# Optimization experiments

Measured on AMD Instinct MI355X. Metric: run time of the kernel, lower is better.

Reference implementation:

```python
import jax, jax.numpy as jnp
import numpy as np

NUM_HEADS = 16
ROPE_THETA = 10000.0


def setup_inputs() -> dict:
    key = jax.random.key(0)
    k1, k2, k3 = jax.random.split(key, 3)
    B, T, C = 2, 2048, 1024
    x = jax.random.normal(k1, (B, T, C), dtype=jnp.float32)
    w_qkv = jax.random.normal(k2, (3 * C, C), dtype=jnp.float32) * 0.02
    w_out = jax.random.normal(k3, (C, C), dtype=jnp.float32) * 0.02
    return {"x": x, "w_qkv": w_qkv, "w_out": w_out}


def _apply_rope(x, cos, sin):
    # x: (B, H, T, D); interleaved complex pairs: (x[...,2i], x[...,2i+1])
    B, H, T, D = x.shape
    xp = x.reshape(B, H, T, D // 2, 2)
    xr, xi = xp[..., 0], xp[..., 1]
    # cos/sin: (T, D//2) broadcast over (B, H)
    out_r = xr * cos - xi * sin
    out_i = xr * sin + xi * cos
    return jnp.stack([out_r, out_i], axis=-1).reshape(B, H, T, D)


def reference(x, w_qkv, w_out):
    B, T, C = x.shape
    H = NUM_HEADS
    D = C // H
    scale = 1.0 / np.sqrt(D).astype(np.float32)

    qkv = x @ w_qkv.T                      # (B, T, 3C)
    q, k, v = jnp.split(qkv, 3, axis=-1)

    def to_heads(t):
        return t.reshape(B, T, H, D).transpose(0, 2, 1, 3)  # (B, H, T, D)

    q, k, v = to_heads(q), to_heads(k), to_heads(v)

    # RoPE frequencies: freqs[t, j] = t / theta^(2j/D)
    inv_freq = 1.0 / (ROPE_THETA ** (jnp.arange(0, D, 2, dtype=jnp.float32) / D))
    freqs = jnp.arange(T, dtype=jnp.float32)[:, None] * inv_freq[None, :]  # (T, D//2)
    cos, sin = jnp.cos(freqs), jnp.sin(freqs)

    q = _apply_rope(q, cos, sin)
    k = _apply_rope(k, cos, sin)

    att = jnp.einsum('bhqd,bhkd->bhqk', q, k) * scale   # (B, H, T, T)
    causal = jnp.tril(jnp.ones((T, T), dtype=bool))
    att = jnp.where(causal[None, None], att, -jnp.inf)
    att = jax.nn.softmax(att, axis=-1)
    # dropout p=0.0 (eval) -> identity

    out = jnp.einsum('bhqk,bhkd->bhqd', att, v)          # (B, H, T, D)
    out = out.transpose(0, 2, 1, 3).reshape(B, T, C)
    return out @ w_out.T
```

## Files before the change

kernel.cpp:

```cpp
#include <hip/hip_runtime.h>
#include <hip/hip_bf16.h>
#include <math.h>

#define DEV __device__ __forceinline__

typedef float  floatx4 __attribute__((ext_vector_type(4)));
typedef short  bf16x8  __attribute__((ext_vector_type(8)));
typedef short  bf16x4  __attribute__((ext_vector_type(4)));

typedef __attribute__((address_space(1))) void gvoid;
typedef __attribute__((address_space(3))) void lvoid;

static constexpr int Bc = 2, Tc = 2048, Cc = 1024, Hc = 16, Dc = 64;

DEV void gload16(const void* g, void* l) {
    __builtin_amdgcn_global_load_lds((gvoid*)g, (lvoid*)l, 16, 0, 0);
}

__global__ void prep_kernel(const float* __restrict__ xf,
                            const float* __restrict__ wqkvf,
                            const float* __restrict__ woutf,
                            __hip_bfloat16* __restrict__ xb,
                            __hip_bfloat16* __restrict__ wqkvb,
                            __hip_bfloat16* __restrict__ woutb,
                            float* __restrict__ cosT, float* __restrict__ sinT) {
    int gb = blockIdx.x;
    if (gb < 8192) {
        const float* src; __hip_bfloat16* dst; int i;
        if (gb < 4096)      { src = xf;    dst = xb;    i = gb * 256 + threadIdx.x; }
        else if (gb < 7168) { src = wqkvf; dst = wqkvb; i = (gb - 4096) * 256 + threadIdx.x; }
        else                { src = woutf; dst = woutb; i = (gb - 7168) * 256 + threadIdx.x; }
        float4 f = ((const float4*)src)[i];
        union { ushort4 u; __hip_bfloat16 h[4]; } pk;
        pk.h[0] = __float2bfloat16(f.x);
        pk.h[1] = __float2bfloat16(f.y);
        pk.h[2] = __float2bfloat16(f.z);
        pk.h[3] = __float2bfloat16(f.w);
        ((ushort4*)dst)[i] = pk.u;
    } else {
        int i = (gb - 8192) * 256 + threadIdx.x;
        int j = i >> 11, t = i & 2047;
        float invf = powf(10000.0f, -(float)j / 32.0f);
        float f = (float)t * invf;
        cosT[i] = cosf(f);
        sinT[i] = sinf(f);
    }
}

__global__ __launch_bounds__(256, 2) void gemm_qkv(
    const __hip_bfloat16* __restrict__ A,
    const __hip_bfloat16* __restrict__ Bm,
    __hip_bfloat16* __restrict__ qb,
    __hip_bfloat16* __restrict__ kb,
    __hip_bfloat16* __restrict__ vb,
    const float* __restrict__ cosT,
    const float* __restrict__ sinT,
    int K)
{
    __shared__ __align__(16) __hip_bfloat16 SM[2 * 128 * 64];
    __hip_bfloat16* const As = SM;
    __hip_bfloat16* const Bs = SM + 128 * 64;

    const int tid  = threadIdx.x;
    const int lane = tid & 63, wave = tid >> 6;
    const int quad = lane >> 4, cidx = lane & 15;
    const int wm = wave & 1, wn = wave >> 1;
    const int bm = blockIdx.x * 128, bn = blockIdx.y * 128;

    floatx4 acc[4][4] = {};

    for (int k0 = 0; k0 < K; k0 += 64) {
#pragma unroll
        for (int it = 0; it < 4; ++it) {
            int idx = tid + it * 256;
            int r = idx >> 3, cs = idx & 7;
            int cg = cs ^ (r & 7);
            gload16(A  + (size_t)(bm + r) * K + k0 + cg * 8, As + idx * 8);
            gload16(Bm + (size_t)(bn + r) * K + k0 + cg * 8, Bs + idx * 8);
        }
        __syncthreads();
#pragma unroll
        for (int ks = 0; ks < 2; ++ks) {
            bf16x8 af[4], bf[4];
#pragma unroll
            for (int mt = 0; mt < 4; ++mt) {
                int r = wm * 64 + mt * 16 + cidx;
                af[mt] = *(const bf16x8*)(As + (r * 8 + ((ks * 4 + quad) ^ (r & 7))) * 8);
            }
#pragma unroll
            for (int nt = 0; nt < 4; ++nt) {
                int r = wn * 64 + nt * 16 + cidx;
                bf[nt] = *(const bf16x8*)(Bs + (r * 8 + ((ks * 4 + quad) ^ (r & 7))) * 8);
            }
#pragma unroll
            for (int mt = 0; mt < 4; ++mt)
#pragma unroll
                for (int nt = 0; nt < 4; ++nt)
                    acc[mt][nt] = __builtin_amdgcn_mfma_f32_16x16x32_bf16(
                        af[mt], bf[nt], acc[mt][nt], 0, 0, 0);
        }
        __syncthreads();
    }

    if (bn >= 2048) {
#pragma unroll
        for (int nt = 0; nt < 4; ++nt) {
            int n_l = wn * 64 + nt * 16 + cidx;
#pragma unroll
            for (int mt = 0; mt < 4; ++mt)
#pragma unroll
                for (int reg = 0; reg < 4; ++reg) {
                    int m_l = wm * 64 + mt * 16 + quad * 4 + reg;
                    SM[n_l * 128 + (((m_l >> 3) ^ (n_l & 15)) * 8) + (m_l & 7)] =
                        __float2bfloat16(acc[mt][nt][reg]);
                }
        }
        __syncthreads();
        {
            int b = bm >> 11, t0 = bm & 2047;
            int c = tid & 15;
#pragma unroll
            for (int it = 0; it < 8; ++it) {
                int row = it * 16 + (tid >> 4);
                int cc = (bn - 2048) + row;
                int h = cc >> 6, d = cc & 63;
                *(uint4*)(vb + ((size_t)(b * Hc + h) * Dc + d) * Tc + t0 + c * 8) =
                    *(const uint4*)(SM + row * 128 + ((c ^ (row & 15)) * 8));
            }
        }
    } else {
        const float SL2E = 0.125f * 1.44269504088896f;
        const bool isq = (bn < 1024);
#pragma unroll
        for (int nt = 0; nt < 4; ++nt) {
            int n_l = wn * 64 + nt * 16 + cidx;
            int d = n_l & 63, j = d >> 1;
            const float* cp = cosT + j * 2048;
            const float* sp = sinT + j * 2048;
#pragma unroll
            for (int mt = 0; mt < 4; ++mt) {
                int m0 = wm * 64 + mt * 16 + quad * 4;
                int t0 = (bm + m0) & 2047;
                float4 c4 = *(const float4*)(cp + t0);
                float4 s4 = *(const float4*)(sp + t0);
#pragma unroll
                for (int reg = 0; reg < 4; ++reg) {
                    float v = acc[mt][nt][reg];
                    float p = __shfl_xor(v, 1);
                    float cz = ((const float*)&c4)[reg];
                    float sz = ((const float*)&s4)[reg];
                    float o = (d & 1) ? (p * sz + v * cz) : (v * cz - p * sz);
                    if (isq) o *= SL2E;
                    int m_l = m0 + reg;
                    SM[m_l * 128 + (((n_l >> 3) ^ (m_l & 15)) * 8) + (n_l & 7)] =
                        __float2bfloat16(o);
                }
            }
        }
        __syncthreads();
        {
            __hip_bfloat16* dst = isq ? qb : kb;
            const int bnl = bn & 1023;
#pragma unroll
            for (int it = 0; it < 8; ++it) {
                int c = it * 256 + tid;
                int row = c >> 4, s = c & 15;
                int m = bm + row;
                int b = m >> 11, t = m & 2047;
                int h = (bnl >> 6) + (s >> 3);
                int d0 = (s & 7) * 8;
                *(uint4*)(dst + ((size_t)(b * Hc + h) * Tc + t) * Dc + d0) =
                    *(const uint4*)(SM + row * 128 + ((s ^ (row & 15)) * 8));
            }
        }
    }
}

__global__ __launch_bounds__(256, 2) void gemm_out(
    const __hip_bfloat16* __restrict__ A,
    const __hip_bfloat16* __restrict__ Bm,
    float* __restrict__ Cout)
{
    __shared__ __align__(16) __hip_bfloat16 As[64 * 64];
    __shared__ __align__(16) __hip_bfloat16 Bs[128 * 64];

    const int tid  = threadIdx.x;
    const int lane = tid & 63, wave = tid >> 6;
    const int quad = lane >> 4, cidx = lane & 15;
    const int bm = blockIdx.x * 64, bn = blockIdx.y * 128;
    const int K = 1024;

    floatx4 acc[4][2] = {};

    for (int k0 = 0; k0 < K; k0 += 64) {
        int h = k0 >> 6;
#pragma unroll
        for (int it = 0; it < 2; ++it) {
            int idx = tid + it * 256;
            int r = idx >> 3, cs = idx & 7;
            int cg = cs ^ (r & 7);
            int m = bm + r;
            const __hip_bfloat16* src =
                A + ((size_t)((m >> 11) * 16 + h) * 2048 + (m & 2047)) * 64 + cg * 8;
            gload16(src, As + idx * 8);
        }
#pragma unroll
        for (int it = 0; it < 4; ++it) {
            int idx = tid + it * 256;
            int r = idx >> 3, cs = idx & 7;
            int cg = cs ^ (r & 7);
            gload16(Bm + (size_t)(bn + r) * K + k0 + cg * 8, Bs + idx * 8);
        }
        __syncthreads();
#pragma unroll
        for (int ks = 0; ks < 2; ++ks) {
            bf16x8 af[4], bf[2];
#pragma unroll
            for (int mt = 0; mt < 4; ++mt) {
                int r = mt * 16 + cidx;
                af[mt] = *(const bf16x8*)(As + (r * 8 + ((ks * 4 + quad) ^ (r & 7))) * 8);
            }
#pragma unroll
            for (int nt = 0; nt < 2; ++nt) {
                int r = wave * 32 + nt * 16 + cidx;
                bf[nt] = *(const bf16x8*)(Bs + (r * 8 + ((ks * 4 + quad) ^ (r & 7))) * 8);
            }
#pragma unroll
            for (int mt = 0; mt < 4; ++mt)
#pragma unroll
                for (int nt = 0; nt < 2; ++nt)
                    acc[mt][nt] = __builtin_amdgcn_mfma_f32_16x16x32_bf16(
                        af[mt], bf[nt], acc[mt][nt], 0, 0, 0);
        }
        __syncthreads();
    }

#pragma unroll
    for (int mt = 0; mt < 4; ++mt)
#pragma unroll
        for (int nt = 0; nt < 2; ++nt) {
            int n = bn + wave * 32 + nt * 16 + cidx;
#pragma unroll
            for (int reg = 0; reg < 4; ++reg) {
                int m = bm + mt * 16 + quad * 4 + reg;
                Cout[(size_t)m * 1024 + n] = acc[mt][nt][reg];
            }
        }
}

__global__ __launch_bounds__(256, 2) void attn_kernel(
    const __hip_bfloat16* __restrict__ qb,
    const __hip_bfloat16* __restrict__ kb,
    const __hip_bfloat16* __restrict__ vb,
    __hip_bfloat16* __restrict__ ob)
{
    __shared__ __align__(16) __hip_bfloat16 KB[2 * 128 * 64];
    __shared__ __align__(16) __hip_bfloat16 VB[2 * 64 * 128];

    const int tid  = threadIdx.x;
    const int lane = tid & 63, wave = tid >> 6;
    const int quad = lane >> 4, cidx = lane & 15;
    const int id = blockIdx.x;
    const int xcd = id & 7, s = id >> 3;
    const int bh  = xcd * 4 + (s & 3);
    const int m   = s >> 2;
    const int qt  = (m < 8) ? (15 - m) : (m - 8);
    const int qbase = qt * 128;
    const int ktmax = qt;
    const size_t plane = (size_t)bh * Tc * Dc;
    const __hip_bfloat16* Vp = vb + plane;
    const __hip_bfloat16* Kp = kb + plane;

    __hip_bfloat16* const Qs = KB + 128 * 64;
    __hip_bfloat16* const Os = KB;

#pragma unroll
    for (int it = 0; it < 4; ++it) {
        int idx = tid + it * 256;
        int r = idx >> 3, cg = (idx & 7) ^ (r & 7);
        gload16(qb + plane + (size_t)(qbase + r) * 64 + cg * 8, Qs + idx * 8);
    }
#pragma unroll
    for (int it = 0; it < 4; ++it) {
        int idx = tid + it * 256;
        int r = idx >> 3, cg = (idx & 7) ^ (r & 7);
        gload16(Kp + (size_t)r * 64 + cg * 8, KB + idx * 8);
    }
#pragma unroll
    for (int it = 0; it < 4; ++it) {
        int idx = tid + it * 256;
        int r = idx >> 4, c = (idx & 15) ^ (r & 15);
        gload16(Vp + (size_t)r * Tc + c * 8, VB + idx * 8);
    }
    __syncthreads();

    bf16x8 qf[2][2];
#pragma unroll
    for (int qb2 = 0; qb2 < 2; ++qb2)
#pragma unroll
        for (int ks = 0; ks < 2; ++ks) {
            int r = wave * 32 + qb2 * 16 + cidx;
            qf[qb2][ks] = *(const bf16x8*)(Qs + (r * 8 + ((ks * 4 + quad) ^ (r & 7))) * 8);
        }
    __syncthreads();

    floatx4 oaccT[2][4] = {};
    floatx4 lpart[2] = {};
    const int q0 = qbase + wave * 32 + cidx;

    for (int kt = 0; kt <= ktmax; ++kt) {
        const __hip_bfloat16* Kc = KB + (kt & 1) * (128 * 64);
        const __hip_bfloat16* Vc = VB + (kt & 1) * (64 * 128);

        if (kt < ktmax) {
            __hip_bfloat16* Kn = KB + ((kt + 1) & 1) * (128 * 64);
            __hip_bfloat16* Vn = VB + ((kt + 1) & 1) * (64 * 128);
#pragma unroll
            for (int it = 0; it < 4; ++it) {
                int idx = tid + it * 256;
                int r = idx >> 3, cg = (idx & 7) ^ (r & 7);
                gload16(Kp + (size_t)((kt + 1) * 128 + r) * 64 + cg * 8, Kn + idx * 8);
            }
#pragma unroll
            for (int it = 0; it < 4; ++it) {
                int idx = tid + it * 256;
                int r = idx >> 4, c = (idx & 15) ^ (r & 15);
                gload16(Vp + (size_t)r * Tc + (kt + 1) * 128 + c * 8, Vn + idx * 8);
            }
        }

        floatx4 sacc[2][8] = {};
#pragma unroll
        for (int ks = 0; ks < 2; ++ks)
#pragma unroll
            for (int kb8 = 0; kb8 < 8; ++kb8) {
                int r = kb8 * 16 + cidx;
                bf16x8 af = *(const bf16x8*)(
                    Kc + (r * 8 + ((ks * 4 + quad) ^ (r & 7))) * 8);
                sacc[0][kb8] = __builtin_amdgcn_mfma_f32_16x16x32_bf16(
                    af, qf[0][ks], sacc[0][kb8], 0, 0, 0);
                sacc[1][kb8] = __builtin_amdgcn_mfma_f32_16x16x32_bf16(
                    af, qf[1][ks], sacc[1][kb8], 0, 0, 0);
            }

        const bool domask = (kt == ktmax);
        bf16x4 pf[2][8];
#pragma unroll
        for (int qb2 = 0; qb2 < 2; ++qb2) {
            const int q = q0 + qb2 * 16;
#pragma unroll
            for (int kb8 = 0; kb8 < 8; ++kb8)
#pragma unroll
                for (int reg = 0; reg < 4; ++reg) {
                    int key = kt * 128 + kb8 * 16 + quad * 4 + reg;
                    float p = __builtin_amdgcn_exp2f(sacc[qb2][kb8][reg]);
                    if (domask && key > q) p = 0.0f;
                    lpart[qb2][reg] += p;
                    __hip_bfloat16 hb = __float2bfloat16(p);
                    pf[qb2][kb8][reg] = *(const short*)&hb;
                }
        }

#pragma unroll
        for (int dt = 0; dt < 4; ++dt) {
            int d = dt * 16 + cidx;
#pragma unroll
            for (int c8 = 0; c8 < 8; ++c8) {
                int ch = c8 * 2 + (quad >> 1);
                bf16x4 vtf = *(const bf16x4*)(
                    Vc + (d * 16 + (ch ^ (d & 15))) * 8 + (quad & 1) * 4);
                oaccT[0][dt] = __builtin_amdgcn_mfma_f32_16x16x16bf16_1k(
                    vtf, pf[0][c8], oaccT[0][dt], 0, 0, 0);
                oaccT[1][dt] = __builtin_amdgcn_mfma_f32_16x16x16bf16_1k(
                    vtf, pf[1][c8], oaccT[1][dt], 0, 0, 0);
            }
        }

        __syncthreads();
    }

#pragma unroll
    for (int qb2 = 0; qb2 < 2; ++qb2) {
        float l = lpart[qb2][0] + lpart[qb2][1] + lpart[qb2][2] + lpart[qb2][3];
        l += __shfl_xor(l, 16);
        l += __shfl_xor(l, 32);
        float inv = 1.0f / l;
        int qq = wave * 32 + qb2 * 16 + cidx;
#pragma unroll
        for (int dt = 0; dt < 4; ++dt) {
            bf16x4 o4;
#pragma unroll
            for (int reg = 0; reg < 4; ++reg) {
                __hip_bfloat16 hb = __float2bfloat16(oaccT[qb2][dt][reg] * inv);
                o4[reg] = *(const short*)&hb;
            }
            int g = dt * 4 + quad;
            *(bf16x4*)(Os + qq * 64 + ((g ^ (qq & 12)) * 4)) = o4;
        }
    }
    __syncthreads();
#pragma unroll
    for (int i = 0; i < 4; ++i) {
        int c = tid + i * 256;
        int row = c >> 3, cp = c & 7;
        *(uint4*)(ob + plane + (size_t)(qbase + row) * 64 + cp * 8) =
            *(const uint4*)(Os + row * 64 + ((cp * 2) ^ (row & 12)) * 4);
    }
}

extern "C" void kernel_launch(void* const* d_in, const int* in_sizes, int n_in,
                              void* d_out, int out_size, void* d_ws, size_t ws_size,
                              hipStream_t stream) {
    const float* xf = nullptr; const float* wqkvf = nullptr; const float* woutf = nullptr;
    for (int i = 0; i < n_in; ++i) {
        if      (in_sizes[i] == 2 * 2048 * 1024) xf    = (const float*)d_in[i];
        else if (in_sizes[i] == 3 * 1024 * 1024) wqkvf = (const float*)d_in[i];
        else if (in_sizes[i] == 1024 * 1024)     woutf = (const float*)d_in[i];
    }
    float* out = (float*)d_out;

    char* ws = (char*)d_ws;
    const size_t MB = 1024 * 1024;
    __hip_bfloat16* qb    = (__hip_bfloat16*)(ws);
    __hip_bfloat16* kb    = (__hip_bfloat16*)(ws + 8  * MB);
    __hip_bfloat16* vb    = (__hip_bfloat16*)(ws + 16 * MB);
    __hip_bfloat16* ab    = (__hip_bfloat16*)(ws + 24 * MB);
    float* cosT           = (float*)(ws + 32 * MB);
    float* sinT           = (float*)(ws + 32 * MB + 256 * 1024);
    __hip_bfloat16* xb    = (__hip_bfloat16*)(ws + 33 * MB);
    __hip_bfloat16* wqkvb = (__hip_bfloat16*)(ws + 41 * MB);
    __hip_bfloat16* woutb = (__hip_bfloat16*)(ws + 47 * MB);

    prep_kernel<<<dim3(8448), dim3(256), 0, stream>>>(
        xf, wqkvf, woutf, xb, wqkvb, woutb, cosT, sinT);

    gemm_qkv<<<dim3(32, 24), dim3(256), 0, stream>>>(
        xb, wqkvb, qb, kb, vb, cosT, sinT, 1024);
    attn_kernel<<<dim3(512), dim3(256), 0, stream>>>(qb, kb, vb, ab);
    gemm_out<<<dim3(64, 8), dim3(256), 0, stream>>>(ab, woutb, out);
}
```

Baseline: 162.7 us.

## Restructure QKV GEMM into 256x256 tiles with double-buffered phased loads

The QKV projection GEMM now uses 512-thread blocks computing 256x256 tiles with 8 waves, instead of 256-thread blocks on 128x128 tiles. LDS tiles are double-buffered, and the next K-slice is loaded in four phases interleaved with the MFMA work, using explicit vmcnt waits, raw barriers and setprio. The epilogue is rewritten so each wave stages and writes its own 128x64 slab, which removes the block-wide syncs. The intent is to hide global-load latency and improve operand reuse; the cost is 64KB of LDS, higher register pressure (8x4 accumulators) and only 192 blocks, which may underfill the 256 CUs.

```diff
diff --git a/kernel.cpp b/kernel.cpp
--- a/kernel.cpp
+++ b/kernel.cpp
@@ -47,7 +47,7 @@
     }
 }
 
-__global__ __launch_bounds__(256, 2) void gemm_qkv(
+__global__ __launch_bounds__(512, 1) void gemm_qkv(
     const __hip_bfloat16* __restrict__ A,
     const __hip_bfloat16* __restrict__ Bm,
     __hip_bfloat16* __restrict__ qb,
@@ -57,120 +57,187 @@
     const float* __restrict__ sinT,
     int K)
 {
-    __shared__ __align__(16) __hip_bfloat16 SM[2 * 128 * 64];
-    __hip_bfloat16* const As = SM;
-    __hip_bfloat16* const Bs = SM + 128 * 64;
+    __shared__ __align__(16) __hip_bfloat16 SA[2 * 256 * 64];
+    __shared__ __align__(16) __hip_bfloat16 SB[2 * 256 * 64];
 
     const int tid  = threadIdx.x;
     const int lane = tid & 63, wave = tid >> 6;
     const int quad = lane >> 4, cidx = lane & 15;
-    const int wm = wave & 1, wn = wave >> 1;
-    const int bm = blockIdx.x * 128, bn = blockIdx.y * 128;
-
-    floatx4 acc[4][4] = {};
-
-    for (int k0 = 0; k0 < K; k0 += 64) {
-#pragma unroll
-        for (int it = 0; it < 4; ++it) {
-            int idx = tid + it * 256;
-            int r = idx >> 3, cs = idx & 7;
-            int cg = cs ^ (r & 7);
-            gload16(A  + (size_t)(bm + r) * K + k0 + cg * 8, As + idx * 8);
-            gload16(Bm + (size_t)(bn + r) * K + k0 + cg * 8, Bs + idx * 8);
-        }
-        __syncthreads();
-#pragma unroll
-        for (int ks = 0; ks < 2; ++ks) {
-            bf16x8 af[4], bf[4];
-#pragma unroll
-            for (int mt = 0; mt < 4; ++mt) {
-                int r = wm * 64 + mt * 16 + cidx;
-                af[mt] = *(const bf16x8*)(As + (r * 8 + ((ks * 4 + quad) ^ (r & 7))) * 8);
-            }
-#pragma unroll
-            for (int nt = 0; nt < 4; ++nt) {
+    const int wm = wave >> 2, wn = wave & 3;
+    const int bm = blockIdx.x * 256, bn = blockIdx.y * 256;
+    const int NT = K >> 6;
+
+    floatx4 acc[8][4] = {};
+
+#pragma unroll
+    for (int j = 0; j < 4; ++j) {
+        int c = tid + j * 512;
+        int r = c >> 3, cg = (c & 7) ^ (r & 7);
+        gload16(A  + (size_t)(bm + r) * K + cg * 8, SA + c * 8);
+    }
+#pragma unroll
+    for (int j = 0; j < 4; ++j) {
+        int c = tid + j * 512;
+        int r = c >> 3, cg = (c & 7) ^ (r & 7);
+        gload16(Bm + (size_t)(bn + r) * K + cg * 8, SB + c * 8);
+    }
+
+    for (int t = 0; t < NT; ++t) {
+        const int p = t & 1;
+        const __hip_bfloat16* Ab = SA + p * (256 * 64);
+        const __hip_bfloat16* Bb = SB + p * (256 * 64);
+        __hip_bfloat16* An = SA + (p ^ 1) * (256 * 64);
+        __hip_bfloat16* Bn = SB + (p ^ 1) * (256 * 64);
+        const int k1 = (t + 1) * 64;
+        const bool more = (t < NT - 1);
+
+        bf16x8 bfr[4][2];
+        bf16x8 afr[2][2];
+
+        if (more) {
+#pragma unroll
+            for (int j = 0; j < 2; ++j) {
+                int c = tid + j * 512;
+                int r = c >> 3, cg = (c & 7) ^ (r & 7);
+                gload16(A + (size_t)(bm + r) * K + k1 + cg * 8, An + c * 8);
+            }
+            asm volatile("s_waitcnt vmcnt(2)" ::: "memory");
+        } else {
+            asm volatile("s_waitcnt vmcnt(0)" ::: "memory");
+        }
+        __builtin_amdgcn_sched_barrier(0);
+        __builtin_amdgcn_s_barrier();
+
+#pragma unroll
+        for (int nt = 0; nt < 4; ++nt)
+#pragma unroll
+            for (int ks = 0; ks < 2; ++ks) {
                 int r = wn * 64 + nt * 16 + cidx;
-                bf[nt] = *(const bf16x8*)(Bs + (r * 8 + ((ks * 4 + quad) ^ (r & 7))) * 8);
-            }
-#pragma unroll
-            for (int mt = 0; mt < 4; ++mt)
+                bfr[nt][ks] = *(const bf16x8*)(Bb + (r * 8 + ((ks * 4 + quad) ^ (r & 7))) * 8);
+            }
+#pragma unroll
+        for (int ms = 0; ms < 2; ++ms)
+#pragma unroll
+            for (int ks = 0; ks < 2; ++ks) {
+                int r = wm * 128 + ms * 16 + cidx;
+                afr[ms][ks] = *(const bf16x8*)(Ab + (r * 8 + ((ks * 4 + quad) ^ (r & 7))) * 8);
+            }
+        __builtin_amdgcn_s_setprio(1);
+#pragma unroll
+        for (int ks = 0; ks < 2; ++ks)
+#pragma unroll
+            for (int ms = 0; ms < 2; ++ms)
 #pragma unroll
                 for (int nt = 0; nt < 4; ++nt)
-                    acc[mt][nt] = __builtin_amdgcn_mfma_f32_16x16x32_bf16(
-                        af[mt], bf[nt], acc[mt][nt], 0, 0, 0);
-        }
-        __syncthreads();
-    }
-
-    if (bn >= 2048) {
-#pragma unroll
-        for (int nt = 0; nt < 4; ++nt) {
-            int n_l = wn * 64 + nt * 16 + cidx;
-#pragma unroll
-            for (int mt = 0; mt < 4; ++mt)
-#pragma unroll
-                for (int reg = 0; reg < 4; ++reg) {
-                    int m_l = wm * 64 + mt * 16 + quad * 4 + reg;
-                    SM[n_l * 128 + (((m_l >> 3) ^ (n_l & 15)) * 8) + (m_l & 7)] =
-                        __float2bfloat16(acc[mt][nt][reg]);
+                    acc[ms][nt] = __builtin_amdgcn_mfma_f32_16x16x32_bf16(
+                        afr[ms][ks], bfr[nt][ks], acc[ms][nt], 0, 0, 0);
+        __builtin_amdgcn_s_setprio(0);
+        __builtin_amdgcn_s_barrier();
+
+#pragma unroll
+        for (int ph = 1; ph < 4; ++ph) {
+            if (more) {
+                const __hip_bfloat16* g = (ph < 2) ? A : Bm;
+                const int rowoff = (ph < 2) ? bm : bn;
+                __hip_bfloat16* dstb = (ph < 2) ? An : Bn;
+                const int hbase = (ph & 1) * 1024;
+#pragma unroll
+                for (int j = 0; j < 2; ++j) {
+                    int c = hbase + tid + j * 512;
+                    int r = c >> 3, cg = (c & 7) ^ (r & 7);
+                    gload16(g + (size_t)(rowoff + r) * K + k1 + cg * 8, dstb + c * 8);
                 }
-        }
-        __syncthreads();
-        {
-            int b = bm >> 11, t0 = bm & 2047;
-            int c = tid & 15;
-#pragma unroll
-            for (int it = 0; it < 8; ++it) {
-                int row = it * 16 + (tid >> 4);
-                int cc = (bn - 2048) + row;
-                int h = cc >> 6, d = cc & 63;
-                *(uint4*)(vb + ((size_t)(b * Hc + h) * Dc + d) * Tc + t0 + c * 8) =
-                    *(const uint4*)(SM + row * 128 + ((c ^ (row & 15)) * 8));
-            }
-        }
-    } else {
+            }
+#pragma unroll
+            for (int ms = 0; ms < 2; ++ms)
+#pragma unroll
+                for (int ks = 0; ks < 2; ++ks) {
+                    int r = wm * 128 + (ph * 2 + ms) * 16 + cidx;
+                    afr[ms][ks] = *(const bf16x8*)(Ab + (r * 8 + ((ks * 4 + quad) ^ (r & 7))) * 8);
+                }
+            __builtin_amdgcn_s_barrier();
+            __builtin_amdgcn_s_setprio(1);
+#pragma unroll
+            for (int ks = 0; ks < 2; ++ks)
+#pragma unroll
+                for (int ms = 0; ms < 2; ++ms)
+#pragma unroll
+                    for (int nt = 0; nt < 4; ++nt)
+                        acc[ph * 2 + ms][nt] = __builtin_amdgcn_mfma_f32_16x16x32_bf16(
+                            afr[ms][ks], bfr[nt][ks], acc[ph * 2 + ms][nt], 0, 0, 0);
+            __builtin_amdgcn_s_setprio(0);
+            __builtin_amdgcn_s_barrier();
+        }
+    }
+
+    __hip_bfloat16* ws = ((wave < 4) ? SA : SB) + (wave & 3) * 8192;
+    const int b = bm >> 11;
+
+    if (bn < 2048) {
         const float SL2E = 0.125f * 1.44269504088896f;
         const bool isq = (bn < 1024);
+        const int h = ((bn & 1023) >> 6) + wn;
 #pragma unroll
         for (int nt = 0; nt < 4; ++nt) {
-            int n_l = wn * 64 + nt * 16 + cidx;
-            int d = n_l & 63, j = d >> 1;
+            int n_l = nt * 16 + cidx;
+            int d = n_l, j = d >> 1;
             const float* cp = cosT + j * 2048;
             const float* sp = sinT + j * 2048;
 #pragma unroll
-            for (int mt = 0; mt < 4; ++mt) {
-                int m0 = wm * 64 + mt * 16 + quad * 4;
+            for (int mt = 0; mt < 8; ++mt) {
+                int m0 = wm * 128 + mt * 16 + quad * 4;
                 int t0 = (bm + m0) & 2047;
                 float4 c4 = *(const float4*)(cp + t0);
                 float4 s4 = *(const float4*)(sp + t0);
 #pragma unroll
                 for (int reg = 0; reg < 4; ++reg) {
                     float v = acc[mt][nt][reg];
-                    float p = __shfl_xor(v, 1);
+                    float pr = __shfl_xor(v, 1);
                     float cz = ((const float*)&c4)[reg];
                     float sz = ((const float*)&s4)[reg];
-                    float o = (d & 1) ? (p * sz + v * cz) : (v * cz - p * sz);
+                    float o = (d & 1) ? (pr * sz + v * cz) : (v * cz - pr * sz);
                     if (isq) o *= SL2E;
-                    int m_l = m0 + reg;
-                    SM[m_l * 128 + (((n_l >> 3) ^ (m_l & 15)) * 8) + (n_l & 7)] =
+                    int r_l = mt * 16 + quad * 4 + reg;
+                    ws[r_l * 64 + (((n_l >> 3) ^ (r_l & 7)) * 8) + (n_l & 7)] =
                         __float2bfloat16(o);
                 }
             }
         }
-        __syncthreads();
         {
             __hip_bfloat16* dst = isq ? qb : kb;
-            const int bnl = bn & 1023;
-#pragma unroll
-            for (int it = 0; it < 8; ++it) {
-                int c = it * 256 + tid;
-                int row = c >> 4, s = c & 15;
-                int m = bm + row;
-                int b = m >> 11, t = m & 2047;
-                int h = (bnl >> 6) + (s >> 3);
-                int d0 = (s & 7) * 8;
-                *(uint4*)(dst + ((size_t)(b * Hc + h) * Tc + t) * Dc + d0) =
-                    *(const uint4*)(SM + row * 128 + ((s ^ (row & 15)) * 8));
+#pragma unroll
+            for (int it = 0; it < 16; ++it) {
+                int c = lane + it * 64;
+                int row = c >> 3, cp8 = c & 7;
+                int m = bm + wm * 128 + row;
+                int tt = m & 2047;
+                *(uint4*)(dst + ((size_t)(b * Hc + h) * Tc + tt) * Dc + cp8 * 8) =
+                    *(const uint4*)(ws + row * 64 + ((cp8 ^ (row & 7)) * 8));
+            }
+        }
+    } else {
+        const int cc0 = (bn - 2048) + wn * 64;
+        const int h = cc0 >> 6;
+#pragma unroll
+        for (int nt = 0; nt < 4; ++nt) {
+            int d_l = nt * 16 + cidx;
+#pragma unroll
+            for (int mt = 0; mt < 8; ++mt)
+#pragma unroll
+                for (int reg = 0; reg < 4; ++reg) {
+                    int t_l = mt * 16 + quad * 4 + reg;
+                    ws[d_l * 128 + (((t_l >> 3) ^ (d_l & 15)) * 8) + (t_l & 7)] =
+                        __float2bfloat16(acc[mt][nt][reg]);
+                }
+        }
+        {
+            int t0 = (bm + wm * 128) & 2047;
+#pragma unroll
+            for (int it = 0; it < 16; ++it) {
+                int c = lane + it * 64;
+                int row = c >> 4, cp16 = c & 15;
+                *(uint4*)(vb + ((size_t)(b * Hc + h) * Dc + row) * Tc + t0 + cp16 * 8) =
+                    *(const uint4*)(ws + row * 128 + ((cp16 ^ (row & 15)) * 8));
             }
         }
     }
@@ -434,7 +501,7 @@
     prep_kernel<<<dim3(8448), dim3(256), 0, stream>>>(
         xf, wqkvf, woutf, xb, wqkvb, woutb, cosT, sinT);
 
-    gemm_qkv<<<dim3(32, 24), dim3(256), 0, stream>>>(
+    gemm_qkv<<<dim3(16, 12), dim3(512), 0, stream>>>(
         xb, wqkvb, qb, kb, vb, cosT, sinT, 1024);
     attn_kernel<<<dim3(512), dim3(256), 0, stream>>>(qb, kb, vb, ab);
     gemm_out<<<dim3(64, 8), dim3(256), 0, stream>>>(ab, woutb, out);
```

New measurement: 191.9 us. 1.18x slower.
